# Kernel tuning notes

Measured on AMD Instinct MI355X. Metric: run time of the kernel, lower is better.

Reference implementation:

```python
import jax, jax.numpy as jnp
import numpy as np

N_GRAPHS = 32
NODES_PER_GRAPH = 512
N = N_GRAPHS * NODES_PER_GRAPH
DEG = 32
E = N * DEG
D = 128
HID = 256
NEXP = 8
EHID = 64
L = 3
CUTOFF = 10.0
ROUTE_W = 0.1


def _graph_norm(x, seg, w, b, ms, num, eps=1e-5):
    # PyG GraphNorm: x - mean_scale*mean_per_graph, normalized by per-graph std
    cnt = jax.ops.segment_sum(jnp.ones((x.shape[0],), x.dtype), seg, num_segments=num)[:, None]
    mean = jax.ops.segment_sum(x, seg, num_segments=num) / cnt
    out = x - ms * mean[seg]
    var = jax.ops.segment_sum(out * out, seg, num_segments=num) / cnt
    std = jnp.sqrt(var + eps)
    return w * out / std[seg] + b


def setup_inputs() -> dict:
    key = jax.random.key(0)
    ks = jax.random.split(key, 8)
    rng = np.random.default_rng(0)
    # radius-graph surrogate: each node gathers DEG in-graph neighbors
    tgt = np.repeat(np.arange(N), DEG)
    src = (tgt // NODES_PER_GRAPH) * NODES_PER_GRAPH + rng.integers(0, NODES_PER_GRAPH, size=E)
    edge_index = jnp.asarray(np.stack([src, tgt]), dtype=jnp.int32)
    batch = jnp.asarray(np.arange(N) // NODES_PER_GRAPH, dtype=jnp.int32)
    atom_type = jax.random.randint(ks[0], (N,), 0, 200, dtype=jnp.int32)
    pos = jax.random.uniform(ks[1], (N, 3), jnp.float32) * 5.0  # box side 5 -> dist < CUTOFF
    s = 0.1
    emb = jax.random.normal(ks[2], (200, D), jnp.float32) * s
    edge_w1 = jax.random.normal(ks[3], (L, 1, EHID), jnp.float32) * s
    edge_b1 = jnp.zeros((L, EHID), jnp.float32)
    edge_w2 = jax.random.normal(ks[4], (L, EHID, NEXP), jnp.float32) * s
    edge_b2 = jnp.zeros((L, NEXP), jnp.float32)
    node_w1 = jax.random.normal(ks[5], (L, NEXP, D, HID), jnp.float32) * s
    node_b1 = jnp.zeros((L, NEXP, HID), jnp.float32)
    node_w2 = jax.random.normal(ks[6], (L, NEXP, HID, D), jnp.float32) * s
    node_b2 = jnp.zeros((L, NEXP, D), jnp.float32)
    gn_w = jnp.ones((L, D), jnp.float32)
    gn_b = jnp.zeros((L, D), jnp.float32)
    gn_ms = jnp.ones((L, D), jnp.float32)
    dn_w = jnp.ones((1,), jnp.float32)
    dn_b = jnp.zeros((1,), jnp.float32)
    dn_ms = jnp.ones((1,), jnp.float32)
    return dict(pos=pos, emb=emb, edge_w1=edge_w1, edge_b1=edge_b1, edge_w2=edge_w2, edge_b2=edge_b2,
                node_w1=node_w1, node_b1=node_b1, node_w2=node_w2, node_b2=node_b2,
                gn_w=gn_w, gn_b=gn_b, gn_ms=gn_ms, dn_w=dn_w, dn_b=dn_b, dn_ms=dn_ms,
                atom_type=atom_type, edge_index=edge_index, batch=batch)


def reference(pos, emb, edge_w1, edge_b1, edge_w2, edge_b2, node_w1, node_b1, node_w2, node_b2,
              gn_w, gn_b, gn_ms, dn_w, dn_b, dn_ms, atom_type, edge_index, batch):
    src, dst = edge_index[0], edge_index[1]  # message j -> i
    dist = jnp.sqrt(jnp.sum((pos[src] - pos[dst]) ** 2, axis=-1))  # [E]
    ebatch = batch[src]
    edge_attr0 = _graph_norm(dist[:, None], ebatch, dn_w, dn_b, dn_ms, N_GRAPHS)  # [E,1]
    ew = (CUTOFF - dist[:, None]) / CUTOFF  # [E,1]
    h = emb[atom_type]  # [N,D]
    total_lbl = jnp.float32(0.0)
    for l in range(L):
        hid_e = jnp.maximum(edge_attr0 @ edge_w1[l] + edge_b1[l], 0.0)  # [E,EHID]
        ea = jax.nn.softmax(hid_e @ edge_w2[l] + edge_b2[l], axis=-1)  # [E,NEXP]
        total_lbl = total_lbl + jnp.sum(jnp.mean(ea, axis=0) ** 2) * NEXP / L
        eaw = ea * ew  # [E,NEXP] routing weight * distance weight
        x_j = h[src]  # [E,D] gathered once per layer
        out = jnp.zeros((N, D), h.dtype)
        for e in range(NEXP):
            agg = jax.ops.segment_sum(x_j * eaw[:, e:e + 1], dst, num_segments=N)  # [N,D]
            h2 = jnp.maximum(agg @ node_w1[l, e] + node_b1[l, e], 0.0) @ node_w2[l, e] + node_b2[l, e]
            out = out + h2
        h = out
        if l + 1 < L:
            h = jnp.tanh(_graph_norm(h, batch, gn_w[l], gn_b[l], gn_ms[l], N_GRAPHS))
    cnt = jax.ops.segment_sum(jnp.ones((N,), h.dtype), batch, num_segments=N_GRAPHS)[:, None]
    pooled = (jax.ops.segment_sum(h, batch, num_segments=N_GRAPHS) / cnt).mean(-1)  # [G]
    return pooled, total_lbl * ROUTE_W
```

## Files before the change

kernel.cpp:

```cpp
#include <hip/hip_runtime.h>
#include <math.h>

#define NG    32
#define NPG   512
#define NN    16384
#define DEG   32
#define NE    524288
#define EPG   16384
#define DD    128
#define HIDN  256
#define NEXPT 8
#define EHID  64
#define NL    3

typedef __attribute__((ext_vector_type(8))) short bh8;
typedef __attribute__((ext_vector_type(4))) float f4;

__device__ __forceinline__ unsigned short bf16_1(float x) {
  unsigned int u = __float_as_uint(x);
  return (unsigned short)((u + 0x7fffu + ((u >> 16) & 1u)) >> 16);
}
__device__ __forceinline__ unsigned int bf16pair(float a, float b) {
  return (unsigned int)bf16_1(a) | ((unsigned int)bf16_1(b) << 16);
}

__global__ void k_zero(float4* p, int n4) {
  int i = blockIdx.x * 256 + threadIdx.x;
  if (i < n4) p[i] = make_float4(0.f, 0.f, 0.f, 0.f);
}

__global__ void k_tr(const float* __restrict__ in, unsigned short* __restrict__ outp,
                     int M, int N) {
  __shared__ float tile[32][33];
  const float* ip = in + (size_t)blockIdx.z * M * N;
  unsigned short* op = outp + (size_t)blockIdx.z * M * N;
  int t = threadIdx.x;
  int i = t >> 5, j = t & 31;
  int c0 = blockIdx.x * 32, r0 = blockIdx.y * 32;
#pragma unroll
  for (int p = 0; p < 4; ++p)
    tile[i + 8 * p][j] = ip[(size_t)(r0 + i + 8 * p) * N + c0 + j];
  __syncthreads();
#pragma unroll
  for (int p = 0; p < 4; ++p)
    op[(size_t)(c0 + i + 8 * p) * M + r0 + j] = bf16_1(tile[j][i + 8 * p]);
}

__global__ void k_dist(const float* __restrict__ pos, const int* __restrict__ src,
                       const int* __restrict__ dst, float* __restrict__ dist,
                       float* __restrict__ gsum, float* __restrict__ gsq) {
  int e = blockIdx.x * 256 + threadIdx.x;
  int s = src[e], t = dst[e];
  float dx = pos[3 * s]     - pos[3 * t];
  float dy = pos[3 * s + 1] - pos[3 * t + 1];
  float dz = pos[3 * s + 2] - pos[3 * t + 2];
  float d = sqrtf(dx * dx + dy * dy + dz * dz);
  dist[e] = d;
  float s1 = d, s2 = d * d;
  for (int o = 32; o; o >>= 1) { s1 += __shfl_down(s1, o); s2 += __shfl_down(s2, o); }
  __shared__ float r1[4], r2[4];
  int w = threadIdx.x >> 6;
  if ((threadIdx.x & 63) == 0) { r1[w] = s1; r2[w] = s2; }
  __syncthreads();
  if (threadIdx.x == 0) {
    int g = e >> 14;
    atomicAdd(&gsum[g], r1[0] + r1[1] + r1[2] + r1[3]);
    atomicAdd(&gsq[g],  r2[0] + r2[1] + r2[2] + r2[3]);
  }
}

__global__ void k_efin(const float* __restrict__ gsum, const float* __restrict__ gsq,
                       const float* __restrict__ dnw, const float* __restrict__ dnb,
                       const float* __restrict__ dnms, float* __restrict__ ga, float* __restrict__ gb) {
  int g = threadIdx.x;
  if (g < NG) {
    float ms = dnms[0];
    float mean = gsum[g] * (1.f / EPG);
    float var = gsq[g] * (1.f / EPG) - (2.f * ms - ms * ms) * mean * mean;
    float a = dnw[0] * rsqrtf(var + 1e-5f);
    ga[g] = a;
    gb[g] = dnb[0] - a * ms * mean;
  }
}

__global__ void k_embed(const float4* __restrict__ emb, const int* __restrict__ at,
                        float4* __restrict__ h) {
  int gid = blockIdx.x * 256 + threadIdx.x;
  int i = gid >> 5, q = gid & 31;
  h[gid] = emb[at[i] * 32 + q];
}

__global__ void k_edge(const float* __restrict__ dist,
                       const float* __restrict__ ga, const float* __restrict__ gb,
                       const float* __restrict__ ew1, const float* __restrict__ eb1,
                       const float* __restrict__ ew2, const float* __restrict__ eb2,
                       float* __restrict__ eaw, float* __restrict__ part) {
  __shared__ float w1s[EHID], b1s[EHID];
  __shared__ __align__(16) float w2s[EHID * NEXPT];
  __shared__ float b2s[NEXPT];
  int t = threadIdx.x;
  if (t < EHID) { w1s[t] = ew1[t]; b1s[t] = eb1[t]; }
  if (t < NEXPT) b2s[t] = eb2[t];
  for (int j = t; j < EHID * NEXPT; j += 256) w2s[j] = ew2[j];
  __syncthreads();

  int e0 = blockIdx.x * 1024 + t * 4;
  float4 dv = *(const float4*)&dist[e0];
  float dd[4] = {dv.x, dv.y, dv.z, dv.w};
  int g = e0 >> 14;
  float gav = ga[g], gbv = gb[g];
  float a0[4], ewv[4];
#pragma unroll
  for (int j = 0; j < 4; ++j) {
    a0[j] = gav * dd[j] + gbv;
    ewv[j] = (10.0f - dd[j]) * 0.1f;
  }
  float acc[4][NEXPT];
#pragma unroll
  for (int j = 0; j < 4; ++j)
#pragma unroll
    for (int x = 0; x < NEXPT; ++x) acc[j][x] = b2s[x];

  for (int k = 0; k < EHID; ++k) {
    float w1k = w1s[k], b1k = b1s[k];
    float hk[4];
#pragma unroll
    for (int j = 0; j < 4; ++j) hk[j] = fmaxf(a0[j] * w1k + b1k, 0.f);
    float4 wa = *(const float4*)&w2s[k * 8];
    float4 wb = *(const float4*)&w2s[k * 8 + 4];
    float ww[8] = {wa.x, wa.y, wa.z, wa.w, wb.x, wb.y, wb.z, wb.w};
#pragma unroll
    for (int j = 0; j < 4; ++j)
#pragma unroll
      for (int x = 0; x < NEXPT; ++x) acc[j][x] += hk[j] * ww[x];
  }

  float esum[NEXPT] = {0, 0, 0, 0, 0, 0, 0, 0};
#pragma unroll
  for (int j = 0; j < 4; ++j) {
    float m = acc[j][0];
#pragma unroll
    for (int x = 1; x < NEXPT; ++x) m = fmaxf(m, acc[j][x]);
    float p[NEXPT], s = 0.f;
#pragma unroll
    for (int x = 0; x < NEXPT; ++x) { p[x] = __expf(acc[j][x] - m); s += p[x]; }
    float inv = 1.f / s;
    float fw = ewv[j] * inv;
    float4 o0 = {p[0] * fw, p[1] * fw, p[2] * fw, p[3] * fw};
    float4 o1 = {p[4] * fw, p[5] * fw, p[6] * fw, p[7] * fw};
    *(float4*)&eaw[(size_t)(e0 + j) * 8]     = o0;
    *(float4*)&eaw[(size_t)(e0 + j) * 8 + 4] = o1;
#pragma unroll
    for (int x = 0; x < NEXPT; ++x) esum[x] += p[x] * inv;
  }
  for (int o = 32; o; o >>= 1)
#pragma unroll
    for (int x = 0; x < NEXPT; ++x) esum[x] += __shfl_down(esum[x], o);
  __shared__ float ps[4][NEXPT];
  int w = t >> 6;
  if ((t & 63) == 0)
#pragma unroll
    for (int x = 0; x < NEXPT; ++x) ps[w][x] = esum[x];
  __syncthreads();
  if (t < NEXPT) part[blockIdx.x * NEXPT + t] = ps[0][t] + ps[1][t] + ps[2][t] + ps[3][t];
}

__global__ __launch_bounds__(256) void k_agg(const float* __restrict__ h, const int* __restrict__ src,
                      const float* __restrict__ eaw, unsigned short* __restrict__ agg) {
  const int t = threadIdx.x;
  const int s = t >> 5;
  const int lane = t & 31;
  const int i = blockIdx.x * 8 + s;
  __shared__ int ssrc[8][DEG];
  __shared__ __align__(16) float sw[8][DEG][NEXPT];
  const int e0b = blockIdx.x * 8 * DEG;
  ssrc[s][lane] = src[e0b + t];
  {
    const float4* ep = (const float4*)&eaw[(size_t)e0b * 8];
    float4* sp = (float4*)&sw[0][0][0];
    sp[t] = ep[t];
    sp[t + 256] = ep[t + 256];
  }
  __syncthreads();
  f4 acc[NEXPT];
#pragma unroll
  for (int x = 0; x < NEXPT; ++x) acc[x] = (f4)0.f;
#pragma unroll 2
  for (int k = 0; k < DEG; ++k) {
    f4 hv = *(const f4*)&h[(size_t)ssrc[s][k] * 128 + lane * 4];
    f4 w0 = *(const f4*)&sw[s][k][0];
    f4 w1 = *(const f4*)&sw[s][k][4];
    float ww[8] = {w0[0], w0[1], w0[2], w0[3], w1[0], w1[1], w1[2], w1[3]};
#pragma unroll
    for (int x = 0; x < NEXPT; ++x) acc[x] += ww[x] * hv;
  }
#pragma unroll
  for (int x = 0; x < NEXPT; ++x) {
    uint2 pk;
    pk.x = bf16pair(acc[x][0], acc[x][1]);
    pk.y = bf16pair(acc[x][2], acc[x][3]);
    *(uint2*)&agg[((size_t)x * NN + i) * 128 + lane * 4] = pk;
  }
}

__global__ __launch_bounds__(256) void k_mlp(
    const unsigned short* __restrict__ agg,
    const unsigned short* __restrict__ w1t,
    const float* __restrict__ b1g,
    const unsigned short* __restrict__ w2t,
    const float* __restrict__ b2g,
    float* __restrict__ out) {
  __shared__ unsigned short hid[64 * 256];
  char* hb = (char*)hid;
  const int t = threadIdx.x;
  const int w = t >> 6;
  const int l15 = t & 15;
  const int q = (t & 63) >> 4;
  const int i0 = blockIdx.x * 64;

  f4 acc2[2][4];
#pragma unroll
  for (int dt = 0; dt < 2; ++dt)
#pragma unroll
    for (int nt = 0; nt < 4; ++nt) acc2[dt][nt] = (f4)0.f;

  for (int x = 0; x < NEXPT; ++x) {
    f4 acc1[4][4];
#pragma unroll
    for (int ht = 0; ht < 4; ++ht) {
      f4 bb = *(const f4*)&b1g[x * 256 + 64 * w + 16 * ht + 4 * q];
#pragma unroll
      for (int nt = 0; nt < 4; ++nt) acc1[ht][nt] = bb;
    }
#pragma unroll
    for (int ks = 0; ks < 4; ++ks) {
      bh8 afr[4], bfr[4];
#pragma unroll
      for (int ht = 0; ht < 4; ++ht)
        afr[ht] = *(const bh8*)&w1t[((size_t)x * 256 + 64 * w + 16 * ht + l15) * 128 + ks * 32 + q * 8];
#pragma unroll
      for (int nt = 0; nt < 4; ++nt)
        bfr[nt] = *(const bh8*)&agg[((size_t)x * NN + i0 + 16 * nt + l15) * 128 + ks * 32 + q * 8];
#pragma unroll
      for (int ht = 0; ht < 4; ++ht)
#pragma unroll
        for (int nt = 0; nt < 4; ++nt)
          acc1[ht][nt] = __builtin_amdgcn_mfma_f32_16x16x32_bf16(afr[ht], bfr[nt], acc1[ht][nt], 0, 0, 0);
    }
    __syncthreads();
#pragma unroll
    for (int ht = 0; ht < 4; ++ht)
#pragma unroll
      for (int nt = 0; nt < 4; ++nt) {
        int node = 16 * nt + l15;
        int h0 = 64 * w + 16 * ht + 4 * q;
        int byte0 = (node * 512 + h0 * 2) ^ ((node & 7) << 4);
        *(unsigned int*)(hb + byte0) =
            bf16pair(fmaxf(acc1[ht][nt][0], 0.f), fmaxf(acc1[ht][nt][1], 0.f));
        *(unsigned int*)(hb + byte0 + 4) =
            bf16pair(fmaxf(acc1[ht][nt][2], 0.f), fmaxf(acc1[ht][nt][3], 0.f));
      }
    __syncthreads();
#pragma unroll
    for (int ks = 0; ks < 8; ++ks) {
      bh8 a2[2], b2f[4];
#pragma unroll
      for (int dt = 0; dt < 2; ++dt)
        a2[dt] = *(const bh8*)&w2t[((size_t)x * 128 + 32 * w + 16 * dt + l15) * 256 + ks * 32 + q * 8];
#pragma unroll
      for (int nt = 0; nt < 4; ++nt) {
        int node = 16 * nt + l15;
        int byte0 = (node * 512 + ks * 64 + q * 16) ^ ((node & 7) << 4);
        b2f[nt] = *(const bh8*)(hb + byte0);
      }
#pragma unroll
      for (int dt = 0; dt < 2; ++dt)
#pragma unroll
        for (int nt = 0; nt < 4; ++nt)
          acc2[dt][nt] = __builtin_amdgcn_mfma_f32_16x16x32_bf16(a2[dt], b2f[nt], acc2[dt][nt], 0, 0, 0);
    }
#pragma unroll
    for (int dt = 0; dt < 2; ++dt) {
      f4 bb = *(const f4*)&b2g[x * 128 + 32 * w + 16 * dt + 4 * q];
#pragma unroll
      for (int nt = 0; nt < 4; ++nt) acc2[dt][nt] += bb;
    }
  }
#pragma unroll
  for (int dt = 0; dt < 2; ++dt)
#pragma unroll
    for (int nt = 0; nt < 4; ++nt)
      *(f4*)&out[(size_t)(i0 + 16 * nt + l15) * 128 + 32 * w + 16 * dt + 4 * q] = acc2[dt][nt];
}

__global__ void k_gnr(const float* __restrict__ h, float* __restrict__ nsum, float* __restrict__ nsq) {
  int g = blockIdx.x, strip = blockIdx.y;
  int c = threadIdx.x;
  const float* base = h + ((size_t)g * NPG + strip * 64) * 128 + c;
  float s = 0.f, q = 0.f;
  for (int n = 0; n < 64; ++n) { float v = base[(size_t)n * 128]; s += v; q += v * v; }
  atomicAdd(&nsum[g * 128 + c], s);
  atomicAdd(&nsq[g * 128 + c], q);
}

__global__ void k_gnf(const float* __restrict__ nsum, const float* __restrict__ nsq,
                      const float* __restrict__ gw, const float* __restrict__ gbv,
                      const float* __restrict__ gms, float* __restrict__ amul, float* __restrict__ aadd) {
  int idx = blockIdx.x * 256 + threadIdx.x;
  int c = idx & 127;
  float ms = gms[c];
  float mean = nsum[idx] * (1.f / NPG);
  float var = nsq[idx] * (1.f / NPG) - (2.f * ms - ms * ms) * mean * mean;
  float a = gw[c] * rsqrtf(var + 1e-5f);
  amul[idx] = a;
  aadd[idx] = gbv[c] - a * ms * mean;
}

__global__ void k_gna(float* __restrict__ h, const float* __restrict__ amul,
                      const float* __restrict__ aadd) {
  int gid = blockIdx.x * 256 + threadIdx.x;
  int i = gid >> 5, q = gid & 31;
  int g = i >> 9;
  float4 v = *(float4*)&h[(size_t)gid * 4];
  float4 a = *(const float4*)&amul[g * 128 + q * 4];
  float4 b = *(const float4*)&aadd[g * 128 + q * 4];
  v.x = tanhf(a.x * v.x + b.x);
  v.y = tanhf(a.y * v.y + b.y);
  v.z = tanhf(a.z * v.z + b.z);
  v.w = tanhf(a.w * v.w + b.w);
  *(float4*)&h[(size_t)gid * 4] = v;
}

__global__ void k_pool(const float* __restrict__ h, float* __restrict__ outp) {
  int g = blockIdx.x, t = threadIdx.x;
  const float4* base = (const float4*)(h + (size_t)g * NPG * 128);
  float s = 0.f;
  for (int p = 0; p < 64; ++p) { float4 v = base[p * 256 + t]; s += v.x + v.y + v.z + v.w; }
  for (int o = 32; o; o >>= 1) s += __shfl_down(s, o);
  __shared__ float r[4];
  if ((t & 63) == 0) r[t >> 6] = s;
  __syncthreads();
  if (t == 0) outp[g] = (r[0] + r[1] + r[2] + r[3]) * (1.f / (NPG * 128));
}

__global__ void k_lbl(const float* __restrict__ part, float* __restrict__ outp) {
  __shared__ float s[NL * NEXPT];
  int t = threadIdx.x;
  if (t < NL * NEXPT) {
    int l = t >> 3, x = t & 7;
    float acc = 0.f;
    for (int b = 0; b < 512; ++b) acc += part[(size_t)(l * 512 + b) * NEXPT + x];
    s[t] = acc;
  }
  __syncthreads();
  if (t == 0) {
    float lbl = 0.f;
    for (int j = 0; j < NL * NEXPT; ++j) { float m = s[j] * (1.f / NE); lbl += m * m; }
    outp[0] = lbl * ((float)NEXPT / NL) * 0.1f;
  }
}

extern "C" void kernel_launch(void* const* d_in, const int* in_sizes, int n_in,
                              void* d_out, int out_size, void* d_ws, size_t ws_size,
                              hipStream_t stream) {
  (void)in_sizes; (void)n_in; (void)out_size; (void)ws_size;
  const float* pos  = (const float*)d_in[0];
  const float* emb  = (const float*)d_in[1];
  const float* ew1  = (const float*)d_in[2];
  const float* eb1  = (const float*)d_in[3];
  const float* ew2  = (const float*)d_in[4];
  const float* eb2  = (const float*)d_in[5];
  const float* nw1  = (const float*)d_in[6];
  const float* nb1  = (const float*)d_in[7];
  const float* nw2  = (const float*)d_in[8];
  const float* nb2  = (const float*)d_in[9];
  const float* gnw  = (const float*)d_in[10];
  const float* gnb  = (const float*)d_in[11];
  const float* gnms = (const float*)d_in[12];
  const float* dnw  = (const float*)d_in[13];
  const float* dnb  = (const float*)d_in[14];
  const float* dnms = (const float*)d_in[15];
  const int* atom   = (const int*)d_in[16];
  const int* eidx   = (const int*)d_in[17];
  float* out = (float*)d_out;

  char* wsb = (char*)d_ws;
  float* dist = (float*)wsb;                 wsb += sizeof(float) * NE;
  float* eaw  = (float*)wsb;                 wsb += sizeof(float) * (size_t)NE * 8;
  unsigned short* aggb = (unsigned short*)wsb; wsb += sizeof(short) * (size_t)8 * NN * 128;
  unsigned short* w1t  = (unsigned short*)wsb; wsb += sizeof(short) * (size_t)NL * 8 * 256 * 128;
  unsigned short* w2t  = (unsigned short*)wsb; wsb += sizeof(short) * (size_t)NL * 8 * 256 * 128;
  float* hA   = (float*)wsb;                 wsb += sizeof(float) * (size_t)NN * 128;
  float* hB   = (float*)wsb;                 wsb += sizeof(float) * (size_t)NN * 128;
  float* gsum = (float*)wsb;                 wsb += sizeof(float) * NG;
  float* gsq  = (float*)wsb;                 wsb += sizeof(float) * NG;
  float* ga   = (float*)wsb;                 wsb += sizeof(float) * NG;
  float* gb   = (float*)wsb;                 wsb += sizeof(float) * NG;
  float* nsum = (float*)wsb;                 wsb += sizeof(float) * NG * 128;
  float* nsq  = (float*)wsb;                 wsb += sizeof(float) * NG * 128;
  float* amul = (float*)wsb;                 wsb += sizeof(float) * NG * 128;
  float* aadd = (float*)wsb;                 wsb += sizeof(float) * NG * 128;
  float* part = (float*)wsb;                 wsb += sizeof(float) * (size_t)NL * 512 * NEXPT;

  const int* srcA = eidx;
  const int* dstA = eidx + NE;

  k_zero<<<1, 256, 0, stream>>>((float4*)gsum, 16);
  {
    dim3 g1(HIDN / 32, DD / 32, NL * NEXPT);
    k_tr<<<g1, 256, 0, stream>>>(nw1, w1t, DD, HIDN);
    dim3 g2(DD / 32, HIDN / 32, NL * NEXPT);
    k_tr<<<g2, 256, 0, stream>>>(nw2, w2t, HIDN, DD);
  }
  k_dist<<<NE / 256, 256, 0, stream>>>(pos, srcA, dstA, dist, gsum, gsq);
  k_efin<<<1, 64, 0, stream>>>(gsum, gsq, dnw, dnb, dnms, ga, gb);
  k_embed<<<NN * 32 / 256, 256, 0, stream>>>((const float4*)emb, atom, (float4*)hA);

  float* hcur = hA;
  float* hnxt = hB;
  for (int l = 0; l < NL; ++l) {
    k_edge<<<NE / 1024, 256, 0, stream>>>(dist, ga, gb, ew1 + l * EHID, eb1 + l * EHID,
                                          ew2 + (size_t)l * EHID * NEXPT, eb2 + l * NEXPT,
                                          eaw, part + (size_t)l * 512 * NEXPT);
    k_agg<<<NN / 8, 256, 0, stream>>>(hcur, srcA, eaw, aggb);
    k_mlp<<<NN / 64, 256, 0, stream>>>(aggb,
                                       w1t + (size_t)l * 8 * 256 * 128,
                                       nb1 + (size_t)l * 8 * 256,
                                       w2t + (size_t)l * 8 * 256 * 128,
                                       nb2 + (size_t)l * 8 * 128, hnxt);
    if (l + 1 < NL) {
      k_zero<<<8, 256, 0, stream>>>((float4*)nsum, 2048);
      dim3 gr(NG, 8);
      k_gnr<<<gr, 128, 0, stream>>>(hnxt, nsum, nsq);
      k_gnf<<<16, 256, 0, stream>>>(nsum, nsq, gnw + l * 128, gnb + l * 128, gnms + l * 128,
                                    amul, aadd);
      k_gna<<<NN * 32 / 256, 256, 0, stream>>>(hnxt, amul, aadd);
    }
    float* tmp = hcur; hcur = hnxt; hnxt = tmp;
  }
  k_pool<<<NG, 256, 0, stream>>>(hcur, out);
  k_lbl<<<1, 64, 0, stream>>>(part, out + NG);
}
```

Baseline: 499.4 us.

## Split expert MLP work over 8 waves with double-buffered hidden tile

The expert MLP kernel now runs 512 threads (8 waves) per 64-node block instead of 4. Each wave computes half as many hidden and output tiles, which cuts accumulator registers per thread. The hidden activation buffer in shared memory is double-buffered by expert parity, so the barrier before writing the hidden tile can go and one sync per expert is saved. In exchange, LDS per block doubles to 64KB, which may limit how many blocks fit per CU, and each agg fragment is now loaded by twice as many waves.

```diff
diff --git a/kernel.cpp b/kernel.cpp
--- a/kernel.cpp
+++ b/kernel.cpp
@@ -203,14 +203,14 @@
   }
 }
 
-__global__ __launch_bounds__(256) void k_mlp(
+__global__ __launch_bounds__(512) void k_mlp(
     const unsigned short* __restrict__ agg,
     const unsigned short* __restrict__ w1t,
     const float* __restrict__ b1g,
     const unsigned short* __restrict__ w2t,
     const float* __restrict__ b2g,
     float* __restrict__ out) {
-  __shared__ unsigned short hid[64 * 256];
+  __shared__ unsigned short hid[2][64 * 256];
   char* hb = (char*)hid;
   const int t = threadIdx.x;
   const int w = t >> 6;
@@ -218,43 +218,41 @@
   const int q = (t & 63) >> 4;
   const int i0 = blockIdx.x * 64;
 
-  f4 acc2[2][4];
-#pragma unroll
-  for (int dt = 0; dt < 2; ++dt)
-#pragma unroll
-    for (int nt = 0; nt < 4; ++nt) acc2[dt][nt] = (f4)0.f;
+  f4 acc2[4];
+#pragma unroll
+  for (int nt = 0; nt < 4; ++nt) acc2[nt] = (f4)0.f;
 
   for (int x = 0; x < NEXPT; ++x) {
-    f4 acc1[4][4];
-#pragma unroll
-    for (int ht = 0; ht < 4; ++ht) {
-      f4 bb = *(const f4*)&b1g[x * 256 + 64 * w + 16 * ht + 4 * q];
+    const int bufb = (x & 1) * 32768;
+    f4 acc1[2][4];
+#pragma unroll
+    for (int ht = 0; ht < 2; ++ht) {
+      f4 bb = *(const f4*)&b1g[x * 256 + 32 * w + 16 * ht + 4 * q];
 #pragma unroll
       for (int nt = 0; nt < 4; ++nt) acc1[ht][nt] = bb;
     }
 #pragma unroll
     for (int ks = 0; ks < 4; ++ks) {
-      bh8 afr[4], bfr[4];
-#pragma unroll
-      for (int ht = 0; ht < 4; ++ht)
-        afr[ht] = *(const bh8*)&w1t[((size_t)x * 256 + 64 * w + 16 * ht + l15) * 128 + ks * 32 + q * 8];
+      bh8 afr[2], bfr[4];
+#pragma unroll
+      for (int ht = 0; ht < 2; ++ht)
+        afr[ht] = *(const bh8*)&w1t[((size_t)x * 256 + 32 * w + 16 * ht + l15) * 128 + ks * 32 + q * 8];
 #pragma unroll
       for (int nt = 0; nt < 4; ++nt)
         bfr[nt] = *(const bh8*)&agg[((size_t)x * NN + i0 + 16 * nt + l15) * 128 + ks * 32 + q * 8];
 #pragma unroll
-      for (int ht = 0; ht < 4; ++ht)
+      for (int ht = 0; ht < 2; ++ht)
 #pragma unroll
         for (int nt = 0; nt < 4; ++nt)
           acc1[ht][nt] = __builtin_amdgcn_mfma_f32_16x16x32_bf16(afr[ht], bfr[nt], acc1[ht][nt], 0, 0, 0);
     }
-    __syncthreads();
-#pragma unroll
-    for (int ht = 0; ht < 4; ++ht)
+#pragma unroll
+    for (int ht = 0; ht < 2; ++ht)
 #pragma unroll
       for (int nt = 0; nt < 4; ++nt) {
         int node = 16 * nt + l15;
-        int h0 = 64 * w + 16 * ht + 4 * q;
-        int byte0 = (node * 512 + h0 * 2) ^ ((node & 7) << 4);
+        int h0 = 32 * w + 16 * ht + 4 * q;
+        int byte0 = bufb + ((node * 512 + h0 * 2) ^ ((node & 7) << 4));
         *(unsigned int*)(hb + byte0) =
             bf16pair(fmaxf(acc1[ht][nt][0], 0.f), fmaxf(acc1[ht][nt][1], 0.f));
         *(unsigned int*)(hb + byte0 + 4) =
@@ -263,34 +261,27 @@
     __syncthreads();
 #pragma unroll
     for (int ks = 0; ks < 8; ++ks) {
-      bh8 a2[2], b2f[4];
-#pragma unroll
-      for (int dt = 0; dt < 2; ++dt)
-        a2[dt] = *(const bh8*)&w2t[((size_t)x * 128 + 32 * w + 16 * dt + l15) * 256 + ks * 32 + q * 8];
+      bh8 a2, b2f[4];
+      a2 = *(const bh8*)&w2t[((size_t)x * 128 + 16 * w + l15) * 256 + ks * 32 + q * 8];
 #pragma unroll
       for (int nt = 0; nt < 4; ++nt) {
         int node = 16 * nt + l15;
-        int byte0 = (node * 512 + ks * 64 + q * 16) ^ ((node & 7) << 4);
+        int byte0 = bufb + ((node * 512 + ks * 64 + q * 16) ^ ((node & 7) << 4));
         b2f[nt] = *(const bh8*)(hb + byte0);
       }
 #pragma unroll
-      for (int dt = 0; dt < 2; ++dt)
-#pragma unroll
-        for (int nt = 0; nt < 4; ++nt)
-          acc2[dt][nt] = __builtin_amdgcn_mfma_f32_16x16x32_bf16(a2[dt], b2f[nt], acc2[dt][nt], 0, 0, 0);
+      for (int nt = 0; nt < 4; ++nt)
+        acc2[nt] = __builtin_amdgcn_mfma_f32_16x16x32_bf16(a2, b2f[nt], acc2[nt], 0, 0, 0);
     }
-#pragma unroll
-    for (int dt = 0; dt < 2; ++dt) {
-      f4 bb = *(const f4*)&b2g[x * 128 + 32 * w + 16 * dt + 4 * q];
-#pragma unroll
-      for (int nt = 0; nt < 4; ++nt) acc2[dt][nt] += bb;
+    {
+      f4 bb = *(const f4*)&b2g[x * 128 + 16 * w + 4 * q];
+#pragma unroll
+      for (int nt = 0; nt < 4; ++nt) acc2[nt] += bb;
     }
   }
 #pragma unroll
-  for (int dt = 0; dt < 2; ++dt)
-#pragma unroll
-    for (int nt = 0; nt < 4; ++nt)
-      *(f4*)&out[(size_t)(i0 + 16 * nt + l15) * 128 + 32 * w + 16 * dt + 4 * q] = acc2[dt][nt];
+  for (int nt = 0; nt < 4; ++nt)
+    *(f4*)&out[(size_t)(i0 + 16 * nt + l15) * 128 + 16 * w + 4 * q] = acc2[nt];
 }
 
 __global__ void k_gnr(const float* __restrict__ h, float* __restrict__ nsum, float* __restrict__ nsq) {
@@ -423,7 +414,7 @@
                                           ew2 + (size_t)l * EHID * NEXPT, eb2 + l * NEXPT,
                                           eaw, part + (size_t)l * 512 * NEXPT);
     k_agg<<<NN / 8, 256, 0, stream>>>(hcur, srcA, eaw, aggb);
-    k_mlp<<<NN / 64, 256, 0, stream>>>(aggb,
+    k_mlp<<<NN / 64, 512, 0, stream>>>(aggb,
                                        w1t + (size_t)l * 8 * 256 * 128,
                                        nb1 + (size_t)l * 8 * 256,
                                        w2t + (size_t)l * 8 * 256 * 128,
```

Result: no change. 508.9 us (+1.9%).

## Split MLP experts across two grid slices with partial sums and reduce kernel

Applied to the files above, without the earlier changes.

The expert MLP kernel now runs a 2D grid where each block handles four of the eight experts for its 64 nodes. Partial results go to a scratch buffer that reuses the eaw workspace, and a new reduction kernel sums the two halves and adds the combined second-layer bias. The shared hidden buffer is double-buffered by expert parity, which removes one barrier per expert. The aim is more parallelism and occupancy for the MLP stage, at the cost of extra global traffic for the partials, an additional launch, and doubled LDS per block.

```diff
diff --git a/kernel.cpp b/kernel.cpp
--- a/kernel.cpp
+++ b/kernel.cpp
@@ -208,15 +208,16 @@
     const unsigned short* __restrict__ w1t,
     const float* __restrict__ b1g,
     const unsigned short* __restrict__ w2t,
-    const float* __restrict__ b2g,
-    float* __restrict__ out) {
-  __shared__ unsigned short hid[64 * 256];
+    float* __restrict__ part) {
+  __shared__ unsigned short hid[2][64 * 256];
   char* hb = (char*)hid;
   const int t = threadIdx.x;
   const int w = t >> 6;
   const int l15 = t & 15;
   const int q = (t & 63) >> 4;
   const int i0 = blockIdx.x * 64;
+  const int x0 = blockIdx.y * 4;
+  float* pout = part + (size_t)blockIdx.y * NN * 128;
 
   f4 acc2[2][4];
 #pragma unroll
@@ -224,7 +225,9 @@
 #pragma unroll
     for (int nt = 0; nt < 4; ++nt) acc2[dt][nt] = (f4)0.f;
 
-  for (int x = 0; x < NEXPT; ++x) {
+  for (int xi = 0; xi < 4; ++xi) {
+    const int x = x0 + xi;
+    const int bufb = (xi & 1) * 32768;
     f4 acc1[4][4];
 #pragma unroll
     for (int ht = 0; ht < 4; ++ht) {
@@ -247,14 +250,13 @@
         for (int nt = 0; nt < 4; ++nt)
           acc1[ht][nt] = __builtin_amdgcn_mfma_f32_16x16x32_bf16(afr[ht], bfr[nt], acc1[ht][nt], 0, 0, 0);
     }
-    __syncthreads();
 #pragma unroll
     for (int ht = 0; ht < 4; ++ht)
 #pragma unroll
       for (int nt = 0; nt < 4; ++nt) {
         int node = 16 * nt + l15;
         int h0 = 64 * w + 16 * ht + 4 * q;
-        int byte0 = (node * 512 + h0 * 2) ^ ((node & 7) << 4);
+        int byte0 = bufb + ((node * 512 + h0 * 2) ^ ((node & 7) << 4));
         *(unsigned int*)(hb + byte0) =
             bf16pair(fmaxf(acc1[ht][nt][0], 0.f), fmaxf(acc1[ht][nt][1], 0.f));
         *(unsigned int*)(hb + byte0 + 4) =
@@ -270,7 +272,7 @@
 #pragma unroll
       for (int nt = 0; nt < 4; ++nt) {
         int node = 16 * nt + l15;
-        int byte0 = (node * 512 + ks * 64 + q * 16) ^ ((node & 7) << 4);
+        int byte0 = bufb + ((node * 512 + ks * 64 + q * 16) ^ ((node & 7) << 4));
         b2f[nt] = *(const bh8*)(hb + byte0);
       }
 #pragma unroll
@@ -279,18 +281,28 @@
         for (int nt = 0; nt < 4; ++nt)
           acc2[dt][nt] = __builtin_amdgcn_mfma_f32_16x16x32_bf16(a2[dt], b2f[nt], acc2[dt][nt], 0, 0, 0);
     }
-#pragma unroll
-    for (int dt = 0; dt < 2; ++dt) {
-      f4 bb = *(const f4*)&b2g[x * 128 + 32 * w + 16 * dt + 4 * q];
-#pragma unroll
-      for (int nt = 0; nt < 4; ++nt) acc2[dt][nt] += bb;
-    }
   }
 #pragma unroll
   for (int dt = 0; dt < 2; ++dt)
 #pragma unroll
     for (int nt = 0; nt < 4; ++nt)
-      *(f4*)&out[(size_t)(i0 + 16 * nt + l15) * 128 + 32 * w + 16 * dt + 4 * q] = acc2[dt][nt];
+      *(f4*)&pout[(size_t)(i0 + 16 * nt + l15) * 128 + 32 * w + 16 * dt + 4 * q] = acc2[dt][nt];
+}
+
+__global__ void k_red(const float4* __restrict__ part, float4* __restrict__ outp,
+                      const float* __restrict__ b2g) {
+  int i = blockIdx.x * 256 + threadIdx.x;
+  int d4 = i & 31;
+  float4 b = make_float4(0.f, 0.f, 0.f, 0.f);
+#pragma unroll
+  for (int x = 0; x < NEXPT; ++x) {
+    float4 bv = *(const float4*)&b2g[x * 128 + d4 * 4];
+    b.x += bv.x; b.y += bv.y; b.z += bv.z; b.w += bv.w;
+  }
+  float4 a0 = part[i];
+  float4 a1 = part[i + NN * 128 / 4];
+  float4 r = {a0.x + a1.x + b.x, a0.y + a1.y + b.y, a0.z + a1.z + b.z, a0.w + a1.w + b.w};
+  outp[i] = r;
 }
 
 __global__ void k_gnr(const float* __restrict__ h, float* __restrict__ nsum, float* __restrict__ nsq) {
@@ -402,6 +414,8 @@
   float* aadd = (float*)wsb;                 wsb += sizeof(float) * NG * 128;
   float* part = (float*)wsb;                 wsb += sizeof(float) * (size_t)NL * 512 * NEXPT;
 
+  float* mpart = eaw;
+
   const int* srcA = eidx;
   const int* dstA = eidx + NE;
 
@@ -423,11 +437,16 @@
                                           ew2 + (size_t)l * EHID * NEXPT, eb2 + l * NEXPT,
                                           eaw, part + (size_t)l * 512 * NEXPT);
     k_agg<<<NN / 8, 256, 0, stream>>>(hcur, srcA, eaw, aggb);
-    k_mlp<<<NN / 64, 256, 0, stream>>>(aggb,
-                                       w1t + (size_t)l * 8 * 256 * 128,
-                                       nb1 + (size_t)l * 8 * 256,
-                                       w2t + (size_t)l * 8 * 256 * 128,
-                                       nb2 + (size_t)l * 8 * 128, hnxt);
+    {
+      dim3 gm(NN / 64, 2);
+      k_mlp<<<gm, 256, 0, stream>>>(aggb,
+                                    w1t + (size_t)l * 8 * 256 * 128,
+                                    nb1 + (size_t)l * 8 * 256,
+                                    w2t + (size_t)l * 8 * 256 * 128,
+                                    mpart);
+    }
+    k_red<<<NN * 128 / 4 / 256, 256, 0, stream>>>((const float4*)mpart, (float4*)hnxt,
+                                                  nb2 + (size_t)l * 8 * 128);
     if (l + 1 < NL) {
       k_zero<<<8, 256, 0, stream>>>((float4*)nsum, 2048);
       dim3 gr(NG, 8);
```

After: 492.7 us. About the same (-1.3%).
